# Kernel optimization log

Hardware: AMD Instinct MI355X
Metric: run time of the kernel (lower is better)

## Reference

```python
import jax, jax.numpy as jnp
import numpy as np

N, E = 50000, 800000
IN, HID, HEADS = 64, 32, 4


def setup_inputs() -> dict:
    key = jax.random.key(0)
    ks = jax.random.split(key, 18)
    x = jax.random.normal(ks[0], (N, IN), jnp.float32)
    edge_index = jax.random.randint(ks[1], (2, E), 0, N)

    def lin(k, fan_in, fan_out):
        kw, kb = jax.random.split(k)
        bound = 1.0 / np.sqrt(fan_in)
        W = jax.random.uniform(kw, (fan_in, fan_out), jnp.float32, -bound, bound)
        b = jax.random.uniform(kb, (fan_out,), jnp.float32, -bound, bound)
        return W, b

    # layer 1: in=IN, out=HID per head, heads=HEADS, concat=True -> out dim HID*HEADS
    Wq1, bq1 = lin(ks[2], IN, HEADS * HID)
    Wk1, bk1 = lin(ks[3], IN, HEADS * HID)
    Wv1, bv1 = lin(ks[4], IN, HEADS * HID)
    Ws1, bs1 = lin(ks[5], IN, HEADS * HID)  # root/skip lin
    # layer 2: in=HID*HEADS, out=HID, heads=1, concat=False
    IN2 = HID * HEADS
    Wq2, bq2 = lin(ks[6], IN2, HID)
    Wk2, bk2 = lin(ks[7], IN2, HID)
    Wv2, bv2 = lin(ks[8], IN2, HID)
    Ws2, bs2 = lin(ks[9], IN2, HID)
    return dict(x=x, edge_index=edge_index,
                Wq1=Wq1, bq1=bq1, Wk1=Wk1, bk1=bk1, Wv1=Wv1, bv1=bv1, Ws1=Ws1, bs1=bs1,
                Wq2=Wq2, bq2=bq2, Wk2=Wk2, bk2=bk2, Wv2=Wv2, bv2=bv2, Ws2=Ws2, bs2=bs2)


def transformer_conv(x, src, dst, Wq, bq, Wk, bk, Wv, bv, Ws, bs, heads, out_ch, concat):
    """PyG TransformerConv (eval mode, root_weight=True, beta=False)."""
    n = x.shape[0]
    q = (x @ Wq + bq).reshape(n, heads, out_ch)  # [N,H,C]
    k = (x @ Wk + bk).reshape(n, heads, out_ch)
    v = (x @ Wv + bv).reshape(n, heads, out_ch)
    # per-edge attention logits: q_i . k_j / sqrt(C)
    logits = jnp.einsum('ehc,ehc->eh', q[dst], k[src]) / jnp.sqrt(jnp.float32(out_ch))
    # segment softmax over incoming edges of each target node
    m = jax.ops.segment_max(logits, dst, num_segments=n)          # [N,H]
    p = jnp.exp(logits - m[dst])                                   # [E,H]
    denom = jax.ops.segment_sum(p, dst, num_segments=n)            # [N,H]
    alpha = p / denom[dst]                                         # [E,H]
    agg = jax.ops.segment_sum(alpha[:, :, None] * v[src], dst, num_segments=n)  # [N,H,C]
    if concat:
        o = agg.reshape(n, heads * out_ch)
    else:
        o = agg.mean(axis=1)
    return o + x @ Ws + bs


def reference(x, edge_index,
              Wq1, bq1, Wk1, bk1, Wv1, bv1, Ws1, bs1,
              Wq2, bq2, Wk2, bk2, Wv2, bv2, Ws2, bs2):
    src, dst = edge_index[0], edge_index[1]
    h = transformer_conv(x, src, dst, Wq1, bq1, Wk1, bk1, Wv1, bv1, Ws1, bs1,
                         HEADS, HID, True)
    h = jax.nn.elu(h)
    out = transformer_conv(h, src, dst, Wq2, bq2, Wk2, bk2, Wv2, bv2, Ws2, bs2,
                           1, HID, False)
    return out
```

## Files before the change

### kernel.cpp

```cpp
#include <hip/hip_runtime.h>
#include <hip/hip_bf16.h>
#include <hip/hip_fp8.h>

#define N_NODES 50000
#define N_EDGES 800000
#define HB 3125
#define GB1 1563
#define NBS 49

static constexpr float SCALE = 0.17677669529663687f;

typedef __attribute__((ext_vector_type(8))) short bf16x8;
typedef __attribute__((ext_vector_type(4))) float f32x4;
typedef __attribute__((ext_vector_type(2))) float f32x2;
#define MFMA16 __builtin_amdgcn_mfma_f32_16x16x32_bf16

static __device__ inline unsigned short f2bf(float f) {
    __hip_bfloat16 h = __float2bfloat16(f);
    return __builtin_bit_cast(unsigned short, h);
}
static __device__ inline unsigned char f2fp8(float f) {
    __hip_fp8_e4m3 h(f);
    return __builtin_bit_cast(unsigned char, h);
}
static __device__ inline float2 bfpair(unsigned u) {
    return make_float2(__uint_as_float(u << 16),
                       __uint_as_float(u & 0xffff0000u));
}
static __device__ inline float dot8f8(const float* q, uint2 u) {
    f32x2 a = __builtin_amdgcn_cvt_pk_f32_fp8(u.x, false);
    f32x2 b = __builtin_amdgcn_cvt_pk_f32_fp8(u.x, true);
    f32x2 c = __builtin_amdgcn_cvt_pk_f32_fp8(u.y, false);
    f32x2 d = __builtin_amdgcn_cvt_pk_f32_fp8(u.y, true);
    return q[0]*a[0] + q[1]*a[1] + q[2]*b[0] + q[3]*b[1]
         + q[4]*c[0] + q[5]*c[1] + q[6]*d[0] + q[7]*d[1];
}
static __device__ inline float dot8(const float* q, uint4 u) {
    float2 a = bfpair(u.x), b = bfpair(u.y), c = bfpair(u.z), d = bfpair(u.w);
    return q[0]*a.x + q[1]*a.y + q[2]*b.x + q[3]*b.y
         + q[4]*c.x + q[5]*c.y + q[6]*d.x + q[7]*d.y;
}
static __device__ inline void acc8(float* acc, float w, uint4 u) {
    float2 a = bfpair(u.x), b = bfpair(u.y), c = bfpair(u.z), d = bfpair(u.w);
    acc[0] += w*a.x; acc[1] += w*a.y; acc[2] += w*b.x; acc[3] += w*b.y;
    acc[4] += w*c.x; acc[5] += w*c.y; acc[6] += w*d.x; acc[7] += w*d.y;
}
static __device__ inline void unpack8(float* o, uint4 u) {
    float2 a = bfpair(u.x), b = bfpair(u.y), c = bfpair(u.z), d = bfpair(u.w);
    o[0]=a.x; o[1]=a.y; o[2]=b.x; o[3]=b.y; o[4]=c.x; o[5]=c.y; o[6]=d.x; o[7]=d.y;
}
static __device__ inline bf16x8 cvt8(const float* p) {
    float4 f0 = *(const float4*)p;
    float4 f1 = *(const float4*)(p + 4);
    bf16x8 r;
    r[0] = (short)f2bf(f0.x); r[1] = (short)f2bf(f0.y);
    r[2] = (short)f2bf(f0.z); r[3] = (short)f2bf(f0.w);
    r[4] = (short)f2bf(f1.x); r[5] = (short)f2bf(f1.y);
    r[6] = (short)f2bf(f1.z); r[7] = (short)f2bf(f1.w);
    return r;
}


__global__ __launch_bounds__(256) void k_ph(
    const int* __restrict__ dst, int* __restrict__ cnt, int* __restrict__ rank,
    const float* __restrict__ Wq1, const float* __restrict__ Wk1,
    const float* __restrict__ Wv1, const float* __restrict__ Ws1,
    const float* __restrict__ Wq2, const float* __restrict__ Wk2,
    const float* __restrict__ Wv2, const float* __restrict__ Ws2,
    unsigned short* __restrict__ Wf1, unsigned short* __restrict__ Wf2)
{
    if (blockIdx.x < HB) {
        int e = blockIdx.x * 256 + threadIdx.x;
        rank[e] = atomicAdd(&cnt[dst[e]], 1);
        return;
    }
    int id = (blockIdx.x - HB) * 256 + threadIdx.x;
    if (id < 32768) {
        int j = id & 7, l = (id >> 3) & 63, ks = (id >> 9) & 1, nt = (id >> 10) & 7, m = (id >> 13) & 3;
        const float* W = (m == 0) ? Wq1 : (m == 1) ? Wk1 : (m == 2) ? Wv1 : Ws1;
        int k = ks * 32 + ((l >> 4) << 3) + j;
        int c = nt * 16 + (l & 15);
        Wf1[id] = f2bf(W[k * 128 + c]);
    } else if (id < 49152) {
        int id2 = id - 32768;
        int j = id2 & 7, l = (id2 >> 3) & 63, ks = (id2 >> 9) & 3, g = (id2 >> 11) & 7;
        int m = g >> 1, t = g & 1;
        const float* W = (m == 0) ? Wq2 : (m == 1) ? Wk2 : (m == 2) ? Wv2 : Ws2;
        int k = ks * 32 + ((l >> 4) << 3) + j;
        int c = t * 16 + (l & 15);
        Wf2[id2] = f2bf(W[k * 32 + c]);
    }
}


__global__ __launch_bounds__(256) void k_gs(
    const int* __restrict__ cnt, int* __restrict__ row, int* __restrict__ bsum,
    int* __restrict__ boff, int* __restrict__ ctr,
    const float* __restrict__ x, const unsigned short* __restrict__ Wf1,
    const float* __restrict__ bq, const float* __restrict__ bk,
    const float* __restrict__ bv, const float* __restrict__ bs,
    unsigned short* __restrict__ qs1, unsigned char* __restrict__ k8,
    unsigned short* __restrict__ v1, int n)
{
    __shared__ unsigned char smem[4 * 4352];
    if (blockIdx.x >= GB1) {
        __shared__ int wsum[4];
        __shared__ int lastBlk;
        int b = blockIdx.x - GB1;
        int t = threadIdx.x;
        int base = b * 1024 + t * 4;
        int v0 = (base + 0 < n) ? cnt[base + 0] : 0;
        int v1i = (base + 1 < n) ? cnt[base + 1] : 0;
        int v2 = (base + 2 < n) ? cnt[base + 2] : 0;
        int v3 = (base + 3 < n) ? cnt[base + 3] : 0;
        int s = v0 + v1i + v2 + v3;
        int lane = t & 63, wid = t >> 6;
        int sc = s;
#pragma unroll
        for (int d = 1; d < 64; d <<= 1) {
            int o = __shfl_up(sc, d);
            if (lane >= d) sc += o;
        }
        if (lane == 63) wsum[wid] = sc;
        __syncthreads();
        int woff = 0;
        for (int w = 0; w < wid; ++w) woff += wsum[w];
        int excl = woff + sc - s;
        if (base + 0 < n) row[base + 0] = excl;
        if (base + 1 < n) row[base + 1] = excl + v0;
        if (base + 2 < n) row[base + 2] = excl + v0 + v1i;
        if (base + 3 < n) row[base + 3] = excl + v0 + v1i + v2;
        if (t == 255) {
            bsum[b] = woff + sc;
            __threadfence();
            lastBlk = (atomicAdd(ctr, 1) == NBS - 1);
        }
        __syncthreads();
        if (lastBlk && t < 64) {
            __threadfence();
            int v = (t < NBS) ? ((volatile int*)bsum)[t] : 0;
            int sc2 = v;
#pragma unroll
            for (int d = 1; d < 64; d <<= 1) {
                int o = __shfl_up(sc2, d);
                if (t >= d) sc2 += o;
            }
            boff[t] = sc2 - v;
            if (t == (N_NODES >> 10)) row[N_NODES] = N_EDGES - (sc2 - v);
        }
        return;
    }
    int w = threadIdx.x >> 6;
    int l = threadIdx.x & 63;
    int rb = blockIdx.x * 32;
    int lr = l & 15, lk = l >> 4;
    f32x4 acc[2][8];
#pragma unroll
    for (int mt = 0; mt < 2; ++mt)
#pragma unroll
        for (int nt = 0; nt < 8; ++nt) acc[mt][nt] = (f32x4){0.f, 0.f, 0.f, 0.f};
#pragma unroll
    for (int ks = 0; ks < 2; ++ks) {
        bf16x8 a[2];
#pragma unroll
        for (int mt = 0; mt < 2; ++mt) {
            int r = rb + mt * 16 + lr;
            if (r >= n) r = n - 1;
            a[mt] = cvt8(x + (size_t)r * 64 + ks * 32 + lk * 8);
        }
#pragma unroll
        for (int nt = 0; nt < 8; ++nt) {
            bf16x8 b = *(const bf16x8*)(Wf1 + (size_t)((w * 8 + nt) * 1024 + ks * 512 + l * 8));
            acc[0][nt] = MFMA16(a[0], b, acc[0][nt], 0, 0, 0);
            acc[1][nt] = MFMA16(a[1], b, acc[1][nt], 0, 0, 0);
        }
    }
    const float* bptr = (w == 0) ? bq : (w == 1) ? bk : (w == 2) ? bv : bs;
    unsigned char* my = smem + w * 4352;
#pragma unroll
    for (int mt = 0; mt < 2; ++mt) {
        if (w == 1) {
            unsigned char* lb = my;
#pragma unroll
            for (int nt = 0; nt < 8; ++nt) {
                float bias = bptr[nt * 16 + lr];
#pragma unroll
                for (int i = 0; i < 4; ++i)
                    lb[(lk * 4 + i) * 144 + nt * 16 + lr] = f2fp8(acc[mt][nt][i] + bias);
            }
#pragma unroll
            for (int p = 0; p < 4; ++p) {
                int rl = p * 4 + lk;
                int r = rb + mt * 16 + rl;
                if (r < n) {
                    uint2 val = *(const uint2*)(lb + rl * 144 + lr * 8);
                    *(uint2*)(k8 + (size_t)r * 128 + lr * 8) = val;
                }
            }
        } else {
            unsigned short* ls = (unsigned short*)my;
#pragma unroll
            for (int nt = 0; nt < 8; ++nt) {
                float bias = bptr[nt * 16 + lr];
#pragma unroll
                for (int i = 0; i < 4; ++i)
                    ls[(lk * 4 + i) * 136 + nt * 16 + lr] = f2bf(acc[mt][nt][i] + bias);
            }
            unsigned short* outp = (w == 0) ? qs1 : (w == 3) ? qs1 + 128 : v1;
            size_t stride = (w == 2) ? 128 : 256;
#pragma unroll
            for (int p = 0; p < 4; ++p) {
                int rl = p * 4 + lk;
                int r = rb + mt * 16 + rl;
                if (r < n) {
                    uint4 val = *(const uint4*)(ls + rl * 136 + lr * 8);
                    *(uint4*)(outp + (size_t)r * stride + lr * 8) = val;
                }
            }
        }
    }
}


__global__ void k_scat(const int* __restrict__ src, const int* __restrict__ dst,
                       const int* __restrict__ row, const int* __restrict__ boff,
                       const int* __restrict__ rank, int* __restrict__ col) {
    int e = blockIdx.x * 256 + threadIdx.x;
    int de = dst[e];
    col[row[de] + boff[de >> 10] + rank[e]] = src[e];
}


__global__ __launch_bounds__(256) void k_gemm2m(
    const unsigned short* __restrict__ h1b, const unsigned short* __restrict__ Wf2,
    const float* __restrict__ bq, const float* __restrict__ bk,
    const float* __restrict__ bv, const float* __restrict__ bs,
    unsigned short* __restrict__ qs2, unsigned short* __restrict__ kv2, int n)
{
    __shared__ unsigned short lds[4][32][72];
    int w = threadIdx.x >> 6;
    int l = threadIdx.x & 63;
    int half = w & 1;
    int rb = blockIdx.x * 64 + (w >> 1) * 32;
    int lr = l & 15, lk = l >> 4;
    f32x4 acc[2][4];
#pragma unroll
    for (int mt = 0; mt < 2; ++mt)
#pragma unroll
        for (int nt = 0; nt < 4; ++nt) acc[mt][nt] = (f32x4){0.f, 0.f, 0.f, 0.f};
#pragma unroll
    for (int ks = 0; ks < 4; ++ks) {
        bf16x8 a[2];
#pragma unroll
        for (int mt = 0; mt < 2; ++mt) {
            int r = rb + mt * 16 + lr;
            if (r >= n) r = n - 1;
            a[mt] = *(const bf16x8*)(h1b + (size_t)r * 128 + ks * 32 + lk * 8);
        }
#pragma unroll
        for (int nt = 0; nt < 4; ++nt) {
            int g = half * 4 + nt;
            bf16x8 b = *(const bf16x8*)(Wf2 + (size_t)((g * 4 + ks) * 512 + l * 8));
            acc[0][nt] = MFMA16(a[0], b, acc[0][nt], 0, 0, 0);
            acc[1][nt] = MFMA16(a[1], b, acc[1][nt], 0, 0, 0);
        }
    }
#pragma unroll
    for (int nt = 0; nt < 4; ++nt) {
        int g = half * 4 + nt;
        int mat = g >> 1;
        int c = (g * 16 + lr) & 31;
        const float* bp = (mat == 0) ? bq : (mat == 1) ? bk : (mat == 2) ? bv : bs;
        float bias = bp[c];
#pragma unroll
        for (int mt = 0; mt < 2; ++mt)
#pragma unroll
            for (int i = 0; i < 4; ++i)
                lds[w][mt * 16 + lk * 4 + i][nt * 16 + lr] = f2bf(acc[mt][nt][i] + bias);
    }
    unsigned short* outA = (half == 0) ? qs2 : kv2 + 32;
    unsigned short* outB = (half == 0) ? kv2 : qs2 + 32;
    int rl8 = l >> 3, ci = (l & 7) * 4;
#pragma unroll
    for (int p = 0; p < 4; ++p) {
        int rl = p * 8 + rl8;
        int r = rb + rl;
        if (r < n) {
            uint2 va = *(const uint2*)&lds[w][rl][ci];
            *(uint2*)(outA + (size_t)r * 64 + ci) = va;
            uint2 vb = *(const uint2*)&lds[w][rl][32 + ci];
            *(uint2*)(outB + (size_t)r * 64 + ci) = vb;
        }
    }
}


__global__ __launch_bounds__(256) void k_agg1(
    const unsigned short* __restrict__ qs1, const unsigned char* __restrict__ k8,
    const unsigned short* __restrict__ v1,
    const int* __restrict__ row, const int* __restrict__ boff,
    const int* __restrict__ col, uint4* __restrict__ h1b, int n)
{
    int i = blockIdx.x * 4 + (threadIdx.x >> 6);
    if (i >= n) return;
    int lane = threadIdx.x & 63;
    int slot = lane >> 4, w = lane & 15;
    float q[8];
    unpack8(q, *(const uint4*)(qs1 + (size_t)i * 256 + w * 8));
    float acc[8] = {};
    float d = 0.f;
    int s = row[i] + boff[i >> 10];
    int e = row[i + 1] + boff[(i + 1) >> 10];
    for (int t = s; t < e; t += 8) {
        int ta = t + slot, tb = t + 4 + slot;
        bool va = ta < e, vb = tb < e;
        int ja = col[va ? ta : s];
        int jb = col[vb ? tb : s];
        uint2 ka = *(const uint2*)(k8 + (size_t)ja * 128 + w * 8);
        uint2 kb = *(const uint2*)(k8 + (size_t)jb * 128 + w * 8);
        uint4 vA = *(const uint4*)(v1 + (size_t)ja * 128 + w * 8);
        uint4 vB = *(const uint4*)(v1 + (size_t)jb * 128 + w * 8);
        float la = dot8f8(q, ka);
        float lb = dot8f8(q, kb);
        la += __shfl_xor(la, 1);  lb += __shfl_xor(lb, 1);
        la += __shfl_xor(la, 2);  lb += __shfl_xor(lb, 2);
        float wa = va ? __expf(la * SCALE) : 0.f;
        float wb = vb ? __expf(lb * SCALE) : 0.f;
        d += wa + wb;
        acc8(acc, wa, vA);
        acc8(acc, wb, vB);
    }
#pragma unroll
    for (int m = 16; m <= 32; m <<= 1) {
        d += __shfl_xor(d, m);
#pragma unroll
        for (int c = 0; c < 8; ++c) acc[c] += __shfl_xor(acc[c], m);
    }
    if (slot == 0) {
        float inv = (d > 0.f) ? 1.f / d : 0.f;
        float sv[8];
        unpack8(sv, *(const uint4*)(qs1 + (size_t)i * 256 + 128 + w * 8));
        unsigned o[4];
#pragma unroll
        for (int p = 0; p < 4; ++p) {
            float rx = acc[2 * p] * inv + sv[2 * p];
            float ry = acc[2 * p + 1] * inv + sv[2 * p + 1];
            rx = (rx > 0.f) ? rx : expm1f(rx);
            ry = (ry > 0.f) ? ry : expm1f(ry);
            o[p] = ((unsigned)f2bf(ry) << 16) | (unsigned)f2bf(rx);
        }
        h1b[(size_t)i * 16 + w] = make_uint4(o[0], o[1], o[2], o[3]);
    }
}


__global__ __launch_bounds__(256) void k_agg2(
    const unsigned short* __restrict__ qs2, const unsigned short* __restrict__ kv2,
    const int* __restrict__ row, const int* __restrict__ boff,
    const int* __restrict__ col, float* __restrict__ out, int n)
{
    int i = blockIdx.x * 4 + (threadIdx.x >> 6);
    if (i >= n) return;
    int lane = threadIdx.x & 63;
    int slot = lane >> 2, qr = lane & 3;
    float q[8];
    unpack8(q, *(const uint4*)(qs2 + (size_t)i * 64 + qr * 8));
    float acc[8] = {};
    float d = 0.f;
    int s = row[i] + boff[i >> 10];
    int e = row[i + 1] + boff[(i + 1) >> 10];
    for (int t = s; t < e; t += 16) {
        int te = t + slot;
        bool va = te < e;
        int j = col[va ? te : s];
        const unsigned short* p = kv2 + (size_t)j * 64;
        uint4 ku = *(const uint4*)(p + qr * 8);
        uint4 vu = *(const uint4*)(p + 32 + qr * 8);
        float lg = dot8(q, ku);
        lg += __shfl_xor(lg, 1);
        lg += __shfl_xor(lg, 2);
        float wv = va ? __expf(lg * SCALE) : 0.f;
        d += wv;
        acc8(acc, wv, vu);
    }
#pragma unroll
    for (int m = 4; m <= 32; m <<= 1) {
        d += __shfl_xor(d, m);
#pragma unroll
        for (int c = 0; c < 8; ++c) acc[c] += __shfl_xor(acc[c], m);
    }
    if (slot == 0) {
        float inv = (d > 0.f) ? 1.f / d : 0.f;
        float sv[8];
        unpack8(sv, *(const uint4*)(qs2 + (size_t)i * 64 + 32 + qr * 8));
        float4 o0, o1;
        o0.x = acc[0] * inv + sv[0];
        o0.y = acc[1] * inv + sv[1];
        o0.z = acc[2] * inv + sv[2];
        o0.w = acc[3] * inv + sv[3];
        o1.x = acc[4] * inv + sv[4];
        o1.y = acc[5] * inv + sv[5];
        o1.z = acc[6] * inv + sv[6];
        o1.w = acc[7] * inv + sv[7];
        *(float4*)&out[(size_t)i * 32 + qr * 8] = o0;
        *(float4*)&out[(size_t)i * 32 + qr * 8 + 4] = o1;
    }
}


extern "C" void kernel_launch(void* const* d_in, const int* in_sizes, int n_in,
                              void* d_out, int out_size, void* d_ws, size_t ws_size,
                              hipStream_t stream)
{
    const int N = N_NODES, E = N_EDGES;
    const float* x   = (const float*)d_in[0];
    const int* edge  = (const int*)d_in[1];
    const int* src   = edge;
    const int* dst   = edge + E;
    const float* Wq1 = (const float*)d_in[2];  const float* bq1 = (const float*)d_in[3];
    const float* Wk1 = (const float*)d_in[4];  const float* bk1 = (const float*)d_in[5];
    const float* Wv1 = (const float*)d_in[6];  const float* bv1 = (const float*)d_in[7];
    const float* Ws1 = (const float*)d_in[8];  const float* bs1 = (const float*)d_in[9];
    const float* Wq2 = (const float*)d_in[10]; const float* bq2 = (const float*)d_in[11];
    const float* Wk2 = (const float*)d_in[12]; const float* bk2 = (const float*)d_in[13];
    const float* Wv2 = (const float*)d_in[14]; const float* bv2 = (const float*)d_in[15];
    const float* Ws2 = (const float*)d_in[16]; const float* bs2 = (const float*)d_in[17];

    char* ws = (char*)d_ws;
    size_t off = 0;
    auto alloc = [&](size_t bytes) -> void* {
        void* p = ws + off;
        off += (bytes + 255) & ~(size_t)255;
        return p;
    };
    unsigned short* qs1 = (unsigned short*)alloc((size_t)N * 256 * 2);
    unsigned char*  k8  = (unsigned char*)alloc((size_t)N * 128);
    unsigned short* v1  = (unsigned short*)alloc((size_t)N * 128 * 2);
    unsigned short* h1b = (unsigned short*)alloc((size_t)N * 128 * 2);
    unsigned short* qs2 = (unsigned short*)alloc((size_t)N * 64 * 2);
    unsigned short* kv2 = (unsigned short*)alloc((size_t)N * 64 * 2);
    unsigned short* Wf1 = (unsigned short*)alloc(32768 * 2);
    unsigned short* Wf2 = (unsigned short*)alloc(16384 * 2);
    int* row_ptr  = (int*)alloc((size_t)(N + 1) * 4);
    int* cnt      = (int*)alloc((size_t)(N + 64) * 4);
    int* ctr      = cnt + N;
    int* rank     = (int*)alloc((size_t)E * 4);
    int* colb     = (int*)alloc((size_t)E * 4);
    int* bsum     = (int*)alloc(64 * 4);
    int* boff     = (int*)alloc(64 * 4);

    hipMemsetAsync(cnt, 0, (size_t)(N + 64) * 4, stream);
    k_ph<<<HB + 192, 256, 0, stream>>>(dst, cnt, rank,
                                       Wq1, Wk1, Wv1, Ws1, Wq2, Wk2, Wv2, Ws2,
                                       Wf1, Wf2);
    k_gs<<<GB1 + NBS, 256, 0, stream>>>(cnt, row_ptr, bsum, boff, ctr,
                                        x, Wf1, bq1, bk1, bv1, bs1, qs1, k8, v1, N);
    k_scat<<<HB, 256, 0, stream>>>(src, dst, row_ptr, boff, rank, colb);
    k_agg1<<<(N + 3) / 4, 256, 0, stream>>>(qs1, k8, v1, row_ptr, boff, colb, (uint4*)h1b, N);
    k_gemm2m<<<(N + 63) / 64, 256, 0, stream>>>(h1b, Wf2, bq2, bk2, bv2, bs2, qs2, kv2, N);
    k_agg2<<<(N + 3) / 4, 256, 0, stream>>>(qs2, kv2, row_ptr, boff, colb, (float*)d_out, N);
}
```

Measured before the change: 168.1 us.

## Store layer-1 values in FP8 interleaved with keys and use packed float math

Layer-1 V projections are now quantized to FP8 and interleaved with the FP8 keys in a single 256-byte-per-node buffer. Each edge gather in the first aggregation then fetches one 16-byte load instead of separate 8-byte K and 16-byte V loads, which halves V gather traffic. Both aggregation kernels also switch to f32x2 vector arithmetic so the compiler can emit packed FMAs. The cost is lower V precision (FP8 instead of bf16), which may raise error in the attention output.

```diff
diff --git a/kernel.cpp b/kernel.cpp
--- a/kernel.cpp
+++ b/kernel.cpp
@@ -14,6 +14,7 @@
 typedef __attribute__((ext_vector_type(4))) float f32x4;
 typedef __attribute__((ext_vector_type(2))) float f32x2;
 #define MFMA16 __builtin_amdgcn_mfma_f32_16x16x32_bf16
+#define CVT8 __builtin_amdgcn_cvt_pk_f32_fp8
 
 static __device__ inline unsigned short f2bf(float f) {
     __hip_bfloat16 h = __float2bfloat16(f);
@@ -23,31 +24,11 @@
     __hip_fp8_e4m3 h(f);
     return __builtin_bit_cast(unsigned char, h);
 }
-static __device__ inline float2 bfpair(unsigned u) {
-    return make_float2(__uint_as_float(u << 16),
-                       __uint_as_float(u & 0xffff0000u));
-}
-static __device__ inline float dot8f8(const float* q, uint2 u) {
-    f32x2 a = __builtin_amdgcn_cvt_pk_f32_fp8(u.x, false);
-    f32x2 b = __builtin_amdgcn_cvt_pk_f32_fp8(u.x, true);
-    f32x2 c = __builtin_amdgcn_cvt_pk_f32_fp8(u.y, false);
-    f32x2 d = __builtin_amdgcn_cvt_pk_f32_fp8(u.y, true);
-    return q[0]*a[0] + q[1]*a[1] + q[2]*b[0] + q[3]*b[1]
-         + q[4]*c[0] + q[5]*c[1] + q[6]*d[0] + q[7]*d[1];
-}
-static __device__ inline float dot8(const float* q, uint4 u) {
-    float2 a = bfpair(u.x), b = bfpair(u.y), c = bfpair(u.z), d = bfpair(u.w);
-    return q[0]*a.x + q[1]*a.y + q[2]*b.x + q[3]*b.y
-         + q[4]*c.x + q[5]*c.y + q[6]*d.x + q[7]*d.y;
-}
-static __device__ inline void acc8(float* acc, float w, uint4 u) {
-    float2 a = bfpair(u.x), b = bfpair(u.y), c = bfpair(u.z), d = bfpair(u.w);
-    acc[0] += w*a.x; acc[1] += w*a.y; acc[2] += w*b.x; acc[3] += w*b.y;
-    acc[4] += w*c.x; acc[5] += w*c.y; acc[6] += w*d.x; acc[7] += w*d.y;
-}
-static __device__ inline void unpack8(float* o, uint4 u) {
-    float2 a = bfpair(u.x), b = bfpair(u.y), c = bfpair(u.z), d = bfpair(u.w);
-    o[0]=a.x; o[1]=a.y; o[2]=b.x; o[3]=b.y; o[4]=c.x; o[5]=c.y; o[6]=d.x; o[7]=d.y;
+static __device__ inline f32x2 bfp2(unsigned u) {
+    f32x2 r;
+    r[0] = __uint_as_float(u << 16);
+    r[1] = __uint_as_float(u & 0xffff0000u);
+    return r;
 }
 static __device__ inline bf16x8 cvt8(const float* p) {
     float4 f0 = *(const float4*)p;
@@ -99,8 +80,7 @@
     const float* __restrict__ x, const unsigned short* __restrict__ Wf1,
     const float* __restrict__ bq, const float* __restrict__ bk,
     const float* __restrict__ bv, const float* __restrict__ bs,
-    unsigned short* __restrict__ qs1, unsigned char* __restrict__ k8,
-    unsigned short* __restrict__ v1, int n)
+    unsigned short* __restrict__ qs1, unsigned char* __restrict__ kv8, int n)
 {
     __shared__ unsigned char smem[4 * 4352];
     if (blockIdx.x >= GB1) {
@@ -179,7 +159,7 @@
     unsigned char* my = smem + w * 4352;
 #pragma unroll
     for (int mt = 0; mt < 2; ++mt) {
-        if (w == 1) {
+        if (w == 1 || w == 2) {
             unsigned char* lb = my;
 #pragma unroll
             for (int nt = 0; nt < 8; ++nt) {
@@ -188,13 +168,14 @@
                 for (int i = 0; i < 4; ++i)
                     lb[(lk * 4 + i) * 144 + nt * 16 + lr] = f2fp8(acc[mt][nt][i] + bias);
             }
+            int voff = (w == 2) ? 8 : 0;
 #pragma unroll
             for (int p = 0; p < 4; ++p) {
                 int rl = p * 4 + lk;
                 int r = rb + mt * 16 + rl;
                 if (r < n) {
                     uint2 val = *(const uint2*)(lb + rl * 144 + lr * 8);
-                    *(uint2*)(k8 + (size_t)r * 128 + lr * 8) = val;
+                    *(uint2*)(kv8 + (size_t)r * 256 + lr * 16 + voff) = val;
                 }
             }
         } else {
@@ -206,15 +187,14 @@
                 for (int i = 0; i < 4; ++i)
                     ls[(lk * 4 + i) * 136 + nt * 16 + lr] = f2bf(acc[mt][nt][i] + bias);
             }
-            unsigned short* outp = (w == 0) ? qs1 : (w == 3) ? qs1 + 128 : v1;
-            size_t stride = (w == 2) ? 128 : 256;
+            unsigned short* outp = (w == 0) ? qs1 : qs1 + 128;
 #pragma unroll
             for (int p = 0; p < 4; ++p) {
                 int rl = p * 4 + lk;
                 int r = rb + mt * 16 + rl;
                 if (r < n) {
                     uint4 val = *(const uint4*)(ls + rl * 136 + lr * 8);
-                    *(uint4*)(outp + (size_t)r * stride + lr * 8) = val;
+                    *(uint4*)(outp + (size_t)r * 256 + lr * 8) = val;
                 }
             }
         }
@@ -296,8 +276,7 @@
 
 
 __global__ __launch_bounds__(256) void k_agg1(
-    const unsigned short* __restrict__ qs1, const unsigned char* __restrict__ k8,
-    const unsigned short* __restrict__ v1,
+    const unsigned short* __restrict__ qs1, const unsigned char* __restrict__ kv8,
     const int* __restrict__ row, const int* __restrict__ boff,
     const int* __restrict__ col, uint4* __restrict__ h1b, int n)
 {
@@ -305,9 +284,12 @@
     if (i >= n) return;
     int lane = threadIdx.x & 63;
     int slot = lane >> 4, w = lane & 15;
-    float q[8];
-    unpack8(q, *(const uint4*)(qs1 + (size_t)i * 256 + w * 8));
-    float acc[8] = {};
+    f32x2 q2[4];
+    {
+        uint4 qu = *(const uint4*)(qs1 + (size_t)i * 256 + w * 8);
+        q2[0] = bfp2(qu.x); q2[1] = bfp2(qu.y); q2[2] = bfp2(qu.z); q2[3] = bfp2(qu.w);
+    }
+    f32x2 acc2[4] = {};
     float d = 0.f;
     int s = row[i] + boff[i >> 10];
     int e = row[i + 1] + boff[(i + 1) >> 10];
@@ -316,20 +298,36 @@
         bool va = ta < e, vb = tb < e;
         int ja = col[va ? ta : s];
         int jb = col[vb ? tb : s];
-        uint2 ka = *(const uint2*)(k8 + (size_t)ja * 128 + w * 8);
-        uint2 kb = *(const uint2*)(k8 + (size_t)jb * 128 + w * 8);
-        uint4 vA = *(const uint4*)(v1 + (size_t)ja * 128 + w * 8);
-        uint4 vB = *(const uint4*)(v1 + (size_t)jb * 128 + w * 8);
-        float la = dot8f8(q, ka);
-        float lb = dot8f8(q, kb);
+        uint4 A = *(const uint4*)(kv8 + (size_t)ja * 256 + w * 16);
+        uint4 B = *(const uint4*)(kv8 + (size_t)jb * 256 + w * 16);
+        f32x2 pa = CVT8(A.x, false) * q2[0];
+        pa += CVT8(A.x, true)  * q2[1];
+        pa += CVT8(A.y, false) * q2[2];
+        pa += CVT8(A.y, true)  * q2[3];
+        f32x2 pb = CVT8(B.x, false) * q2[0];
+        pb += CVT8(B.x, true)  * q2[1];
+        pb += CVT8(B.y, false) * q2[2];
+        pb += CVT8(B.y, true)  * q2[3];
+        float la = pa[0] + pa[1];
+        float lb = pb[0] + pb[1];
         la += __shfl_xor(la, 1);  lb += __shfl_xor(lb, 1);
         la += __shfl_xor(la, 2);  lb += __shfl_xor(lb, 2);
         float wa = va ? __expf(la * SCALE) : 0.f;
         float wb = vb ? __expf(lb * SCALE) : 0.f;
         d += wa + wb;
-        acc8(acc, wa, vA);
-        acc8(acc, wb, vB);
-    }
+        f32x2 wa2 = (f32x2){wa, wa};
+        f32x2 wb2 = (f32x2){wb, wb};
+        acc2[0] += wa2 * CVT8(A.z, false);
+        acc2[1] += wa2 * CVT8(A.z, true);
+        acc2[2] += wa2 * CVT8(A.w, false);
+        acc2[3] += wa2 * CVT8(A.w, true);
+        acc2[0] += wb2 * CVT8(B.z, false);
+        acc2[1] += wb2 * CVT8(B.z, true);
+        acc2[2] += wb2 * CVT8(B.w, false);
+        acc2[3] += wb2 * CVT8(B.w, true);
+    }
+    float acc[8] = {acc2[0][0], acc2[0][1], acc2[1][0], acc2[1][1],
+                    acc2[2][0], acc2[2][1], acc2[3][0], acc2[3][1]};
 #pragma unroll
     for (int m = 16; m <= 32; m <<= 1) {
         d += __shfl_xor(d, m);
@@ -338,13 +336,13 @@
     }
     if (slot == 0) {
         float inv = (d > 0.f) ? 1.f / d : 0.f;
-        float sv[8];
-        unpack8(sv, *(const uint4*)(qs1 + (size_t)i * 256 + 128 + w * 8));
+        uint4 su = *(const uint4*)(qs1 + (size_t)i * 256 + 128 + w * 8);
+        f32x2 sv[4] = {bfp2(su.x), bfp2(su.y), bfp2(su.z), bfp2(su.w)};
         unsigned o[4];
 #pragma unroll
         for (int p = 0; p < 4; ++p) {
-            float rx = acc[2 * p] * inv + sv[2 * p];
-            float ry = acc[2 * p + 1] * inv + sv[2 * p + 1];
+            float rx = acc[2 * p] * inv + sv[p][0];
+            float ry = acc[2 * p + 1] * inv + sv[p][1];
             rx = (rx > 0.f) ? rx : expm1f(rx);
             ry = (ry > 0.f) ? ry : expm1f(ry);
             o[p] = ((unsigned)f2bf(ry) << 16) | (unsigned)f2bf(rx);
@@ -363,9 +361,12 @@
     if (i >= n) return;
     int lane = threadIdx.x & 63;
     int slot = lane >> 2, qr = lane & 3;
-    float q[8];
-    unpack8(q, *(const uint4*)(qs2 + (size_t)i * 64 + qr * 8));
-    float acc[8] = {};
+    f32x2 q2[4];
+    {
+        uint4 qu = *(const uint4*)(qs2 + (size_t)i * 64 + qr * 8);
+        q2[0] = bfp2(qu.x); q2[1] = bfp2(qu.y); q2[2] = bfp2(qu.z); q2[3] = bfp2(qu.w);
+    }
+    f32x2 acc2[4] = {};
     float d = 0.f;
     int s = row[i] + boff[i >> 10];
     int e = row[i + 1] + boff[(i + 1) >> 10];
@@ -376,13 +377,23 @@
         const unsigned short* p = kv2 + (size_t)j * 64;
         uint4 ku = *(const uint4*)(p + qr * 8);
         uint4 vu = *(const uint4*)(p + 32 + qr * 8);
-        float lg = dot8(q, ku);
+        f32x2 pp = bfp2(ku.x) * q2[0];
+        pp += bfp2(ku.y) * q2[1];
+        pp += bfp2(ku.z) * q2[2];
+        pp += bfp2(ku.w) * q2[3];
+        float lg = pp[0] + pp[1];
         lg += __shfl_xor(lg, 1);
         lg += __shfl_xor(lg, 2);
         float wv = va ? __expf(lg * SCALE) : 0.f;
         d += wv;
-        acc8(acc, wv, vu);
-    }
+        f32x2 w2 = (f32x2){wv, wv};
+        acc2[0] += w2 * bfp2(vu.x);
+        acc2[1] += w2 * bfp2(vu.y);
+        acc2[2] += w2 * bfp2(vu.z);
+        acc2[3] += w2 * bfp2(vu.w);
+    }
+    float acc[8] = {acc2[0][0], acc2[0][1], acc2[1][0], acc2[1][1],
+                    acc2[2][0], acc2[2][1], acc2[3][0], acc2[3][1]};
 #pragma unroll
     for (int m = 4; m <= 32; m <<= 1) {
         d += __shfl_xor(d, m);
@@ -391,17 +402,17 @@
     }
     if (slot == 0) {
         float inv = (d > 0.f) ? 1.f / d : 0.f;
-        float sv[8];
-        unpack8(sv, *(const uint4*)(qs2 + (size_t)i * 64 + 32 + qr * 8));
+        uint4 su = *(const uint4*)(qs2 + (size_t)i * 64 + 32 + qr * 8);
+        f32x2 sv[4] = {bfp2(su.x), bfp2(su.y), bfp2(su.z), bfp2(su.w)};
         float4 o0, o1;
-        o0.x = acc[0] * inv + sv[0];
-        o0.y = acc[1] * inv + sv[1];
-        o0.z = acc[2] * inv + sv[2];
-        o0.w = acc[3] * inv + sv[3];
-        o1.x = acc[4] * inv + sv[4];
-        o1.y = acc[5] * inv + sv[5];
-        o1.z = acc[6] * inv + sv[6];
-        o1.w = acc[7] * inv + sv[7];
+        o0.x = acc[0] * inv + sv[0][0];
+        o0.y = acc[1] * inv + sv[0][1];
+        o0.z = acc[2] * inv + sv[1][0];
+        o0.w = acc[3] * inv + sv[1][1];
+        o1.x = acc[4] * inv + sv[2][0];
+        o1.y = acc[5] * inv + sv[2][1];
+        o1.z = acc[6] * inv + sv[3][0];
+        o1.w = acc[7] * inv + sv[3][1];
         *(float4*)&out[(size_t)i * 32 + qr * 8] = o0;
         *(float4*)&out[(size_t)i * 32 + qr * 8 + 4] = o1;
     }
@@ -434,8 +445,7 @@
         return p;
     };
     unsigned short* qs1 = (unsigned short*)alloc((size_t)N * 256 * 2);
-    unsigned char*  k8  = (unsigned char*)alloc((size_t)N * 128);
-    unsigned short* v1  = (unsigned short*)alloc((size_t)N * 128 * 2);
+    unsigned char*  kv8 = (unsigned char*)alloc((size_t)N * 256);
     unsigned short* h1b = (unsigned short*)alloc((size_t)N * 128 * 2);
     unsigned short* qs2 = (unsigned short*)alloc((size_t)N * 64 * 2);
     unsigned short* kv2 = (unsigned short*)alloc((size_t)N * 64 * 2);
@@ -454,9 +464,9 @@
                                        Wq1, Wk1, Wv1, Ws1, Wq2, Wk2, Wv2, Ws2,
                                        Wf1, Wf2);
     k_gs<<<GB1 + NBS, 256, 0, stream>>>(cnt, row_ptr, bsum, boff, ctr,
-                                        x, Wf1, bq1, bk1, bv1, bs1, qs1, k8, v1, N);
+                                        x, Wf1, bq1, bk1, bv1, bs1, qs1, kv8, N);
     k_scat<<<HB, 256, 0, stream>>>(src, dst, row_ptr, boff, rank, colb);
-    k_agg1<<<(N + 3) / 4, 256, 0, stream>>>(qs1, k8, v1, row_ptr, boff, colb, (uint4*)h1b, N);
+    k_agg1<<<(N + 3) / 4, 256, 0, stream>>>(qs1, kv8, row_ptr, boff, colb, (uint4*)h1b, N);
     k_gemm2m<<<(N + 63) / 64, 256, 0, stream>>>(h1b, Wf2, bq2, bk2, bv2, bs2, qs2, kv2, N);
     k_agg2<<<(N + 3) / 4, 256, 0, stream>>>(qs2, kv2, row_ptr, boff, colb, (float*)d_out, N);
 }
```

New measurement: 163.8 us. 2.6% less time.
